# Kernel tuning notes

Measured on AMD Instinct MI355X. Metric: run time of the kernel, lower is better.

The kernel has to match this reference:

```python
import jax, jax.numpy as jnp
import numpy as np

VOCAB, EMBED, HIDDEN = 50257, 256, 512
BATCH, SEQ = 4, 2048


def posneg(x):
    # max(0,x) - |min(0,x)|  (mathematically the identity, computed as written)
    return jnp.maximum(jnp.zeros_like(x), x) - jnp.abs(jnp.minimum(jnp.zeros_like(x), x))


def setup_inputs() -> dict:
    key = jax.random.key(0)
    ks = jax.random.split(key, 10)
    s = 0.02
    return {
        "token_ids": jax.random.randint(ks[0], (BATCH, SEQ), 0, VOCAB),
        "emb_table": jax.random.normal(ks[1], (VOCAB, EMBED), jnp.float32) * s,
        "W1": jax.random.normal(ks[2], (EMBED, HIDDEN), jnp.float32) * s,
        "b1": jax.random.normal(ks[3], (HIDDEN,), jnp.float32) * s,
        "Wq": jax.random.normal(ks[4], (HIDDEN, HIDDEN), jnp.float32) * s,
        "bq": jax.random.normal(ks[5], (HIDDEN,), jnp.float32) * s,
        "Wk": jax.random.normal(ks[6], (HIDDEN, HIDDEN), jnp.float32) * s,
        "bk": jax.random.normal(ks[7], (HIDDEN,), jnp.float32) * s,
        "Wv": jax.random.normal(ks[8], (HIDDEN, HIDDEN), jnp.float32) * s,
        "bv": jax.random.normal(ks[9], (HIDDEN,), jnp.float32) * s,
    }


def reference(token_ids, emb_table, W1, b1, Wq, bq, Wk, bk, Wv, bv):
    emb = emb_table[token_ids]                      # [B,S,E]
    emb = posneg(emb)
    hidden = posneg(emb) @ W1 + b1                  # [B,S,H]
    hidden = posneg(hidden)
    act = jax.nn.gelu(hidden, approximate=False)
    act = posneg(act)
    q = posneg(act) @ Wq + bq
    k = posneg(act) @ Wk + bk
    v = posneg(act) @ Wv + bv
    q, k, v = posneg(q), posneg(k), posneg(v)
    # scaled_dot_product_attention (single head, hand-rolled)
    q, k = posneg(q), posneg(k)
    scores = jnp.einsum("bsh,bth->bst", q, k)       # [B,S,S]
    scores = posneg(scores) / jnp.sqrt(jnp.float32(q.shape[-1]))
    attn = jax.nn.softmax(scores, axis=-1)
    attn = posneg(attn)
    v = posneg(v)
    out = jnp.einsum("bst,bth->bsh", attn, v)       # [B,S,H]
    return posneg(out)
```

## Files before the change

### kernel.cpp

```cpp
#include <hip/hip_runtime.h>
#include <math.h>


typedef unsigned short u16;
typedef u16   u16x8 __attribute__((ext_vector_type(8)));
typedef short s16x8 __attribute__((ext_vector_type(8)));
typedef float f32x4 __attribute__((ext_vector_type(4)));
typedef float f32x8 __attribute__((ext_vector_type(8)));

static __device__ __forceinline__ u16 f2bf(float f) {
    unsigned u = __builtin_bit_cast(unsigned, f);
    u = (u + 0x7fffu + ((u >> 16) & 1u)) >> 16;
    return (u16)u;
}

static __device__ __forceinline__ void gload_lds16(const u16* g, u16* l) {
    __builtin_amdgcn_global_load_lds(
        (const __attribute__((address_space(1))) void*)g,
        (__attribute__((address_space(3))) void*)l, 16, 0, 0);
}

struct PArgs {
    const float* wsrc[4];
    u16*         wdst[4];
    int          wK[4];
    const float* emb;
    const int*   tok;
    u16*         embB;
};

__launch_bounds__(256)
__global__ void prep_k(PArgs p)
{
    const int z = blockIdx.z;
    if (z < 4) {
        const float* W = p.wsrc[z];
        u16* WT = p.wdst[z];
        const int K = p.wK[z];
        const int c0 = blockIdx.x * 64;
        const int r0 = blockIdx.y * 64;
        if (r0 >= K) return;
        __shared__ float T[64][65];
        const int t = threadIdx.x;
        const int col = t & 63;
        const int rb  = t >> 6;
#pragma unroll
        for (int i = 0; i < 16; ++i)
            T[i * 4 + rb][col] = W[(long)(r0 + i * 4 + rb) * 512 + c0 + col];
        __syncthreads();
#pragma unroll
        for (int i = 0; i < 16; ++i) {
            const int orow = i * 4 + rb;
            WT[(long)(c0 + orow) * K + r0 + col] = f2bf(T[col][orow]);
        }
    } else {
        const int b = (z - 4) * 64 + blockIdx.y * 8 + blockIdx.x;
        const int g = (b & 7) * 128 + (b >> 3);
        const int t = g * 2048 + threadIdx.x * 8;
        const int row = t >> 8;
        const int c8  = t & 255;
        f32x8 v = *(const f32x8*)(p.emb + (long)p.tok[row] * 256 + c8);
        u16x8 o;
#pragma unroll
        for (int j = 0; j < 8; ++j) o[j] = f2bf(v[j]);
        *(u16x8*)(p.embB + (long)row * 256 + c8) = o;
    }
}

struct GArgs {
    const u16* A; const u16* B; const float* bias; void* C;
    float* Cpart;
    float* lsum;
    u16 *qd, *kd, *vTd;
    const float *bq, *bk, *bv;
    int K, lda, ldb, ldc;
    long strA, strB, strC;
    float scale;
};

template <int TM, int NT, int KSUB, int OCC, int EPI, int CMODE,
          bool MX, bool SPLITK, bool XSW>
__launch_bounds__(256, OCC)
__global__ void gemm128(GArgs g)
{
    constexpr int BM  = TM * 32;
    constexpr int BN  = NT * 32;
    constexpr int ASZ = BM * 32;
    constexpr int BSZ = BN * 32;
    constexpr int BK  = 32 * KSUB;
    __shared__ u16 smem[2 * KSUB * (ASZ + BSZ)];
    u16* As = smem;
    u16* Bs = smem + 2 * KSUB * ASZ;

    const int bz    = blockIdx.z;
    const int batch = SPLITK ? (bz >> 1) : bz;
    const int kh    = SPLITK ? (bz & 1) : 0;
    const u16* A = g.A + g.strA * batch + (SPLITK ? kh * 1024 : 0);
    const u16* B = g.B + g.strB * batch + (SPLITK ? kh * 1024 : 0);

    int m0, n0;
    if (XSW) {
        const int lid = blockIdx.y * gridDim.x + blockIdx.x;
        const int xcd = lid & 7;
        const int j   = lid >> 3;
        const int mper = gridDim.y >> 3;
        m0 = (xcd * mper + (j % mper)) * BM;
        n0 = (j / mper) * BN;
    } else {
        m0 = (MX ? blockIdx.x : blockIdx.y) * BM;
        n0 = (MX ? blockIdx.y : blockIdx.x) * BN;
    }

    const int t = threadIdx.x;
    const int w = t >> 6;
    const int lane = t & 63;
    const int quad = lane >> 4;
    const int l16  = lane & 15;
    const int wm = w >> 1, wn = w & 1;

    const int srow = w * 16 + (lane >> 2);
    const int skc  = (lane & 3) * 8;
    const u16* ga = A + (long)(m0 + srow) * g.lda + skc;
    const u16* gb = B + (long)(n0 + srow) * g.ldb + skc;
    const long a64 = (long)64 * g.lda;
    const long b64 = (long)64 * g.ldb;

    auto stage = [&](int buf, int k0) {
#pragma unroll
        for (int s = 0; s < KSUB; ++s) {
            u16* la = As + (buf * KSUB + s) * ASZ + w * 512;
            u16* lb = Bs + (buf * KSUB + s) * BSZ + w * 512;
#pragma unroll
            for (int i = 0; i < TM / 2; ++i)
                gload_lds16(ga + i * a64 + k0 + s * 32, la + i * 2048);
#pragma unroll
            for (int i = 0; i < NT / 2; ++i)
                gload_lds16(gb + i * b64 + k0 + s * 32, lb + i * 2048);
        }
    };

    f32x4 acc[TM][NT] = {};
    const int K = SPLITK ? 1024 : g.K;

    stage(0, 0);
    int cur = 0;
    for (int k0 = 0; k0 < K; k0 += BK) {
        __syncthreads();
        if (k0 + BK < K) stage(cur ^ 1, k0 + BK);

#pragma unroll
        for (int s = 0; s < KSUB; ++s) {
            const u16* as = As + (cur * KSUB + s) * ASZ;
            const u16* bs = Bs + (cur * KSUB + s) * BSZ;
            s16x8 af[TM], bf[NT];
#pragma unroll
            for (int x = 0; x < TM; ++x)
                af[x] = *(const s16x8*)&as[(wm * (TM * 16) + x * 16 + l16) * 32 + quad * 8];
#pragma unroll
            for (int y = 0; y < NT; ++y)
                bf[y] = *(const s16x8*)&bs[(wn * (NT * 16) + y * 16 + l16) * 32 + quad * 8];
#pragma unroll
            for (int x = 0; x < TM; ++x)
#pragma unroll
                for (int y = 0; y < NT; ++y)
                    acc[x][y] = __builtin_amdgcn_mfma_f32_16x16x32_bf16(af[x], bf[y], acc[x][y], 0, 0, 0);
        }
        cur ^= 1;
    }

    if constexpr (CMODE == 2) {
        if (n0 >= 1024) {
            constexpr int TPAD = BM + 8;
            constexpr int TPC  = BM / 8;
            constexpr int CPI  = 256 / TPC;
            static_assert(BN * TPAD <= 2 * KSUB * (ASZ + BSZ), "T fits smem");
            u16* T = smem;
            __syncthreads();
#pragma unroll
            for (int y = 0; y < NT; ++y) {
                const int crel = wn * (NT * 16) + y * 16 + l16;
                const float bval = g.bv[n0 - 1024 + crel];
#pragma unroll
                for (int x = 0; x < TM; ++x)
#pragma unroll
                    for (int r = 0; r < 4; ++r) {
                        const int rrel = wm * (TM * 16) + x * 16 + quad * 4 + r;
                        T[crel * TPAD + rrel] = f2bf(acc[x][y][r] + bval);
                    }
            }
            __syncthreads();
            const int vb  = m0 >> 11;
            const int pos = m0 & 2047;
            u16* dst = g.vTd + (long)vb * (512l * 2048) + (long)(n0 - 1024) * 2048 + pos;
#pragma unroll
            for (int i = 0; i < BN / CPI; ++i) {
                const int c  = i * CPI + (t / TPC);
                const int ms = (t % TPC) * 8;
                *(u16x8*)(dst + (long)c * 2048 + ms) = *(const u16x8*)&T[c * TPAD + ms];
            }
            return;
        }
    }

    float* invp = (float*)smem;
    if constexpr (CMODE == 4) {
        __syncthreads();
        if (t < BM) {
            float l = 0.0f;
#pragma unroll
            for (int j = 0; j < 16; ++j)
                l += g.lsum[(long)j * 8192 + batch * 2048 + m0 + t];
            invp[t] = 1.0f / l;
        }
        __syncthreads();
    }

    float rs[TM][4];
    if (CMODE == 3)
#pragma unroll
        for (int x = 0; x < TM; ++x)
#pragma unroll
            for (int r = 0; r < 4; ++r) rs[x][r] = 0.0f;

#pragma unroll
    for (int y = 0; y < NT; ++y) {
        const int col = n0 + wn * (NT * 16) + y * 16 + l16;
        float bval = 0.0f;
        if (CMODE == 2)
            bval = col < 512 ? g.bq[col] : g.bk[col - 512];
        else if (EPI >= 1)
            bval = g.bias[col];
#pragma unroll
        for (int x = 0; x < TM; ++x) {
#pragma unroll
            for (int r = 0; r < 4; ++r) {
                const int row = m0 + wm * (TM * 16) + x * 16 + quad * 4 + r;
                float v = acc[x][y][r] * g.scale + bval;
                if (EPI == 2) v = 0.5f * v * (1.0f + erff(v * 0.70710678118654752f));
                if (CMODE == 3) {
                    const float e = __expf(v);
                    rs[x][r] += e;
                    ((u16*)g.C + g.strC * batch)[(long)row * g.ldc + col] = f2bf(e);
                } else if (CMODE == 2) {
                    u16* dst = col < 512 ? g.qd : g.kd;
                    dst[(long)row * 512 + (col & 511)] = f2bf(v);
                } else if (CMODE == 4) {
                    ((float*)g.C + g.strC * batch)[(long)row * g.ldc + col] = v * invp[row - m0];
                } else if (SPLITK) {
                    float* dst = kh ? g.Cpart : (float*)g.C;
                    dst[g.strC * batch + (long)row * g.ldc + col] = v;
                } else if (CMODE == 1) {
                    ((float*)g.C + g.strC * batch)[(long)row * g.ldc + col] = v;
                } else {
                    ((u16*)g.C + g.strC * batch)[(long)row * g.ldc + col] = f2bf(v);
                }
            }
        }
    }

    if (CMODE == 3) {
        const int nslot = 2 * (n0 / BN) + wn;
#pragma unroll
        for (int x = 0; x < TM; ++x) {
#pragma unroll
            for (int r = 0; r < 4; ++r) {
                float s = rs[x][r];
                s += __shfl_xor(s, 1, 64);
                s += __shfl_xor(s, 2, 64);
                s += __shfl_xor(s, 4, 64);
                s += __shfl_xor(s, 8, 64);
                if (l16 == 0) {
                    const int row = m0 + wm * (TM * 16) + x * 16 + quad * 4 + r;
                    g.lsum[(long)nslot * 8192 + batch * 2048 + row] = s;
                }
            }
        }
    }
}

extern "C" void kernel_launch(void* const* d_in, const int* in_sizes, int n_in,
                              void* d_out, int out_size, void* d_ws, size_t ws_size,
                              hipStream_t stream)
{
    const int*   tok = (const int*)d_in[0];
    const float* emb = (const float*)d_in[1];
    const float* W1  = (const float*)d_in[2];
    const float* b1  = (const float*)d_in[3];
    const float* Wq  = (const float*)d_in[4];
    const float* bq  = (const float*)d_in[5];
    const float* Wk  = (const float*)d_in[6];
    const float* bk  = (const float*)d_in[7];
    const float* Wv  = (const float*)d_in[8];
    const float* bv  = (const float*)d_in[9];
    float* out = (float*)d_out;

    u16* act   = (u16*)d_out;
    u16* wbase = act + 8192l * 512;
    u16* W1T = wbase;
    u16* WqT = wbase + 131072;
    u16* WkT = WqT + 262144;
    u16* WvT = WkT + 262144;

    char* ws = (char*)d_ws;
    u16* q     = (u16*)(ws);
    u16* k     = (u16*)(ws + (8l  << 20));
    u16* vT    = (u16*)(ws + (16l << 20));
    u16* sc    = (u16*)(ws + (24l << 20));
    float* lsum = (float*)(ws + (56l << 20));
    u16* embB  = sc;

    const dim3 blk(256);
    const float iscl = 0.044194173824159216f;
    const long  TB = 2048l * 512;
    const long  SS = 2048l * 2048;

    PArgs p;
    p.wsrc[0] = W1; p.wsrc[1] = Wq; p.wsrc[2] = Wk; p.wsrc[3] = Wv;
    p.wdst[0] = W1T; p.wdst[1] = WqT; p.wdst[2] = WkT; p.wdst[3] = WvT;
    p.wK[0] = 256; p.wK[1] = 512; p.wK[2] = 512; p.wK[3] = 512;
    p.emb = emb; p.tok = tok; p.embB = embB;
    prep_k<<<dim3(8, 8, 20), blk, 0, stream>>>(p);

    {
        GArgs a = {};
        a.A = embB; a.B = W1T; a.bias = b1; a.C = act;
        a.K = 256; a.lda = 256; a.ldb = 256; a.ldc = 512; a.scale = 1.0f;
        gemm128<2, 4, 2, 2, 2, 0, false, false, true><<<dim3(4, 128, 1), blk, 0, stream>>>(a);
    }
    {
        GArgs a = {};
        a.A = act; a.B = WqT; a.K = 512; a.lda = 512; a.ldb = 512; a.scale = 1.0f;
        a.qd = q; a.kd = k; a.vTd = vT; a.bq = bq; a.bk = bk; a.bv = bv;
        gemm128<4, 4, 2, 2, 0, 2, false, false, true><<<dim3(12, 64, 1), blk, 0, stream>>>(a);
    }
    {
        GArgs a = {};
        a.A = q; a.B = k; a.C = sc; a.lsum = lsum;
        a.K = 512; a.lda = 512; a.ldb = 512; a.ldc = 2048;
        a.strA = TB; a.strB = TB; a.strC = SS; a.scale = iscl;
        gemm128<4, 8, 1, 2, 0, 3, false, false, true><<<dim3(8, 16, 4), blk, 0, stream>>>(a);
    }
    {
        GArgs a = {};
        a.A = sc; a.B = vT; a.C = out; a.lsum = lsum;
        a.K = 2048; a.lda = 2048; a.ldb = 2048; a.ldc = 512;
        a.strA = SS; a.strB = TB; a.strC = TB; a.scale = 1.0f;
        gemm128<4, 4, 4, 1, 0, 4, false, false, true><<<dim3(4, 16, 4), blk, 0, stream>>>(a);
    }
}
```

Before: 185.4 us.

## Add triple-buffered prefetch pipeline with vmcnt waits for the PV GEMM

Adds a PIPE template option that uses three LDS buffers, prefetching two k-tiles ahead. Each iteration waits on an explicit vmcnt so only the oldest stage's loads must land, followed by a single barrier. This replaces the __syncthreads double-buffer loop. The attention-times-V GEMM switches to this path with KSUB reduced from 4 to 2, aiming to hide global-load latency better. The hand-coded vmcnt literals hold only for LPS of 6 or 8, and the change alters the per-barrier work granularity.

Result: no change. 185.2 us (-0.1%).

```diff
diff --git a/kernel.cpp b/kernel.cpp
--- a/kernel.cpp
+++ b/kernel.cpp
@@ -78,7 +78,7 @@
     float scale;
 };
 
-template <int TM, int NT, int KSUB, int OCC, int EPI, int CMODE,
+template <int TM, int NT, int KSUB, int OCC, int PIPE, int EPI, int CMODE,
           bool MX, bool SPLITK, bool XSW>
 __launch_bounds__(256, OCC)
 __global__ void gemm128(GArgs g)
@@ -88,9 +88,13 @@
     constexpr int ASZ = BM * 32;
     constexpr int BSZ = BN * 32;
     constexpr int BK  = 32 * KSUB;
-    __shared__ u16 smem[2 * KSUB * (ASZ + BSZ)];
+    constexpr int NBUF = (PIPE == 1) ? 3 : 2;
+    constexpr int LPS  = (TM / 2 + NT / 2) * KSUB;
+    static_assert(PIPE == 0 || LPS == 6 || LPS == 8,
+                  "PIPE=1 vmcnt literal supports LPS 6 or 8");
+    __shared__ u16 smem[NBUF * KSUB * (ASZ + BSZ)];
     u16* As = smem;
-    u16* Bs = smem + 2 * KSUB * ASZ;
+    u16* Bs = smem + NBUF * KSUB * ASZ;
 
     const int bz    = blockIdx.z;
     const int batch = SPLITK ? (bz >> 1) : bz;
@@ -142,16 +146,11 @@
     f32x4 acc[TM][NT] = {};
     const int K = SPLITK ? 1024 : g.K;
 
-    stage(0, 0);
-    int cur = 0;
-    for (int k0 = 0; k0 < K; k0 += BK) {
-        __syncthreads();
-        if (k0 + BK < K) stage(cur ^ 1, k0 + BK);
-
+    auto compute = [&](int buf) {
 #pragma unroll
         for (int s = 0; s < KSUB; ++s) {
-            const u16* as = As + (cur * KSUB + s) * ASZ;
-            const u16* bs = Bs + (cur * KSUB + s) * BSZ;
+            const u16* as = As + (buf * KSUB + s) * ASZ;
+            const u16* bs = Bs + (buf * KSUB + s) * BSZ;
             s16x8 af[TM], bf[NT];
 #pragma unroll
             for (int x = 0; x < TM; ++x)
@@ -165,7 +164,33 @@
                 for (int y = 0; y < NT; ++y)
                     acc[x][y] = __builtin_amdgcn_mfma_f32_16x16x32_bf16(af[x], bf[y], acc[x][y], 0, 0, 0);
         }
-        cur ^= 1;
+    };
+
+    if constexpr (PIPE == 1) {
+        const int nt = K / BK;
+        stage(0, 0);
+        if (nt > 1) stage(1, BK);
+        for (int tt = 0; tt < nt; ++tt) {
+            if (tt + 1 < nt) {
+                if constexpr (LPS == 6) asm volatile("s_waitcnt vmcnt(6)" ::: "memory");
+                else                    asm volatile("s_waitcnt vmcnt(8)" ::: "memory");
+            } else {
+                asm volatile("s_waitcnt vmcnt(0)" ::: "memory");
+            }
+            __builtin_amdgcn_s_barrier();
+            __builtin_amdgcn_sched_barrier(0);
+            if (tt + 2 < nt) stage((tt + 2) % 3, (tt + 2) * BK);
+            compute(tt % 3);
+        }
+    } else {
+        stage(0, 0);
+        int cur = 0;
+        for (int k0 = 0; k0 < K; k0 += BK) {
+            __syncthreads();
+            if (k0 + BK < K) stage(cur ^ 1, k0 + BK);
+            compute(cur);
+            cur ^= 1;
+        }
     }
 
     if constexpr (CMODE == 2) {
@@ -173,7 +198,7 @@
             constexpr int TPAD = BM + 8;
             constexpr int TPC  = BM / 8;
             constexpr int CPI  = 256 / TPC;
-            static_assert(BN * TPAD <= 2 * KSUB * (ASZ + BSZ), "T fits smem");
+            static_assert(BN * TPAD <= NBUF * KSUB * (ASZ + BSZ), "T fits smem");
             u16* T = smem;
             __syncthreads();
 #pragma unroll
@@ -325,26 +350,26 @@
         GArgs a = {};
         a.A = embB; a.B = W1T; a.bias = b1; a.C = act;
         a.K = 256; a.lda = 256; a.ldb = 256; a.ldc = 512; a.scale = 1.0f;
-        gemm128<2, 4, 2, 2, 2, 0, false, false, true><<<dim3(4, 128, 1), blk, 0, stream>>>(a);
+        gemm128<2, 4, 2, 2, 0, 2, 0, false, false, true><<<dim3(4, 128, 1), blk, 0, stream>>>(a);
     }
     {
         GArgs a = {};
         a.A = act; a.B = WqT; a.K = 512; a.lda = 512; a.ldb = 512; a.scale = 1.0f;
         a.qd = q; a.kd = k; a.vTd = vT; a.bq = bq; a.bk = bk; a.bv = bv;
-        gemm128<4, 4, 2, 2, 0, 2, false, false, true><<<dim3(12, 64, 1), blk, 0, stream>>>(a);
+        gemm128<4, 4, 2, 2, 0, 0, 2, false, false, true><<<dim3(12, 64, 1), blk, 0, stream>>>(a);
     }
     {
         GArgs a = {};
         a.A = q; a.B = k; a.C = sc; a.lsum = lsum;
         a.K = 512; a.lda = 512; a.ldb = 512; a.ldc = 2048;
         a.strA = TB; a.strB = TB; a.strC = SS; a.scale = iscl;
-        gemm128<4, 8, 1, 2, 0, 3, false, false, true><<<dim3(8, 16, 4), blk, 0, stream>>>(a);
+        gemm128<4, 8, 1, 2, 0, 0, 3, false, false, true><<<dim3(8, 16, 4), blk, 0, stream>>>(a);
     }
     {
         GArgs a = {};
         a.A = sc; a.B = vT; a.C = out; a.lsum = lsum;
         a.K = 2048; a.lda = 2048; a.ldb = 2048; a.ldc = 512;
         a.strA = SS; a.strB = TB; a.strC = TB; a.scale = 1.0f;
-        gemm128<4, 4, 4, 1, 0, 4, false, false, true><<<dim3(4, 16, 4), blk, 0, stream>>>(a);
-    }
-}
+        gemm128<4, 4, 2, 1, 1, 0, 4, false, false, true><<<dim3(4, 16, 4), blk, 0, stream>>>(a);
+    }
+}
```
